# Optimization experiments

Hardware: AMD Instinct MI355X
Metric: run time of the kernel (lower is better)

Reference implementation:

```python
import jax, jax.numpy as jnp
import numpy as np
from jax import lax

EPS = 1e-5
BETA = 0.25  # commitment cost

def _conv(x, w, b):
    y = lax.conv_general_dilated(x, w, (1, 1), 'VALID',
                                 dimension_numbers=('NCHW', 'OIHW', 'NCHW'))
    return y + b[None, :, None, None]

def _maxpool2(x):
    return lax.reduce_window(x, -jnp.inf, lax.max, (1, 1, 2, 2), (1, 1, 2, 2), 'VALID')

def _bn(x, scale, bias):
    # training-mode batch norm over (N, H, W)
    mean = jnp.mean(x, axis=(0, 2, 3), keepdims=True)
    var = jnp.var(x, axis=(0, 2, 3), keepdims=True)
    xhat = (x - mean) * lax.rsqrt(var + EPS)
    return xhat * scale[None, :, None, None] + bias[None, :, None, None]

def _vq(z_nchw, codebook):
    # z: [B,32,4,4] -> vectors [B*16, 32]
    B, C, H, W = z_nchw.shape
    z = jnp.transpose(z_nchw, (0, 2, 3, 1)).reshape(-1, C)          # [N, D]
    # squared L2 distances to codebook [K, D]
    d = (jnp.sum(z * z, axis=1, keepdims=True)
         + jnp.sum(codebook * codebook, axis=1)
         - 2.0 * z @ codebook.T)                                    # [N, K]
    idx = jnp.argmin(d, axis=1)                                     # [N]
    q = codebook[idx]                                               # [N, D]
    sg = lax.stop_gradient
    vq_loss = jnp.mean((q - sg(z)) ** 2) + BETA * jnp.mean((sg(q) - z) ** 2)
    q_st = z + sg(q - z)                                            # straight-through
    recon = jnp.transpose(q_st.reshape(B, H, W, C), (0, 3, 1, 2))
    return recon, vq_loss

def setup_inputs() -> dict:
    key = jax.random.key(0)
    ks = jax.random.split(key, 12)
    f = lambda k, shape, s: (jax.random.normal(k, shape, jnp.float32) * s)
    inp = {
        'x': jax.random.normal(ks[0], (2048, 3, 32, 32), jnp.float32),
        'conv1_w': f(ks[1], (64, 3, 3, 3), 0.1), 'conv1_b': jnp.zeros((64,), jnp.float32),
        'bn1_scale': jnp.ones((64,), jnp.float32), 'bn1_bias': jnp.zeros((64,), jnp.float32),
        'conv2_w': f(ks[2], (32, 64, 3, 3), 0.05), 'conv2_b': jnp.zeros((32,), jnp.float32),
        'bn2_scale': jnp.ones((32,), jnp.float32), 'bn2_bias': jnp.zeros((32,), jnp.float32),
        'conv3_w': f(ks[3], (32, 32, 3, 3), 0.06), 'conv3_b': jnp.zeros((32,), jnp.float32),
        'bn3_scale': jnp.ones((32,), jnp.float32), 'bn3_bias': jnp.zeros((32,), jnp.float32),
        'codebook': f(ks[4], (100, 32), 0.5),
        'fc1_w': f(ks[5], (64, 512), 0.04), 'fc1_b': jnp.zeros((64,), jnp.float32),
        'fc2_w': f(ks[6], (10, 64), 0.12), 'fc2_b': jnp.zeros((10,), jnp.float32),
    }
    return inp

def reference(x, conv1_w, conv1_b, bn1_scale, bn1_bias,
              conv2_w, conv2_b, bn2_scale, bn2_bias,
              conv3_w, conv3_b, bn3_scale, bn3_bias,
              codebook, fc1_w, fc1_b, fc2_w, fc2_b):
    h = _bn(jax.nn.relu(_maxpool2(_conv(x, conv1_w, conv1_b))), bn1_scale, bn1_bias)
    h = _bn(jax.nn.relu(_maxpool2(_conv(h, conv2_w, conv2_b))), bn2_scale, bn2_bias)
    h = _bn(jax.nn.relu(_conv(h, conv3_w, conv3_b)), bn3_scale, bn3_bias)   # [B,32,4,4]
    recon, vq_loss = _vq(h, codebook)
    blended = 0.5 * recon + h
    flat = blended.reshape(-1, 4 * 4 * 32)
    z1 = jax.nn.relu(flat @ fc1_w.T + fc1_b)
    y = z1 @ fc2_w.T + fc2_b
    return recon, h, vq_loss, jax.nn.log_softmax(y, axis=1)
```

## Files before the change

kernel.cpp:

```cpp
#include <hip/hip_runtime.h>
#include <math.h>


#define CNT1 460800.0
#define CNT2 73728.0
#define CNT3 32768.0

template<int CB, int W4, int J0, int CNT>
__device__ __forceinline__ void conv1_seg(const float* img, const float* wr,
                                          int prow, float bias, float* vout)
{
  float acc[CNT][4];
#pragma unroll
  for (int j = 0; j < CNT; ++j) { acc[j][0] = 0; acc[j][1] = 0; acc[j][2] = 0; acc[j][3] = 0; }
#pragma unroll
  for (int cin = 0; cin < 3; ++cin) {
    float pt[4][4 * W4];
    const float4* src = (const float4*)&img[cin * 1024 + (2 * prow) * 32 + CB];
#pragma unroll
    for (int r = 0; r < 4; ++r)
#pragma unroll
      for (int u = 0; u < W4; ++u) {
        float4 f = src[r * 8 + u];
        pt[r][u * 4 + 0] = f.x; pt[r][u * 4 + 1] = f.y;
        pt[r][u * 4 + 2] = f.z; pt[r][u * 4 + 3] = f.w;
      }
#pragma unroll
    for (int jj = 0; jj < CNT; ++jj) {
      const int c0 = 2 * (J0 + jj) - CB;
#pragma unroll
      for (int kh = 0; kh < 3; ++kh)
#pragma unroll
        for (int kw = 0; kw < 3; ++kw) {
          const float w_ = wr[cin * 9 + kh * 3 + kw];
          acc[jj][0] += pt[kh][c0 + kw] * w_;
          acc[jj][1] += pt[kh][c0 + 1 + kw] * w_;
          acc[jj][2] += pt[kh + 1][c0 + kw] * w_;
          acc[jj][3] += pt[kh + 1][c0 + 1 + kw] * w_;
        }
    }
  }
#pragma unroll
  for (int jj = 0; jj < CNT; ++jj) {
    float v = fmaxf(fmaxf(acc[jj][0], acc[jj][1]), fmaxf(acc[jj][2], acc[jj][3])) + bias;
    vout[J0 + jj] = fmaxf(v, 0.f);
  }
}

__global__ __launch_bounds__(256) void k1_conv1(
    const float* __restrict__ x, const float* __restrict__ w1,
    const float* __restrict__ b1, double* __restrict__ dstats,
    float* __restrict__ y1)
{
  __shared__ float img[3072];
  __shared__ float red_s[256], red_q[256];
  const int n = blockIdx.x, t = threadIdx.x;
  const float4* xin = (const float4*)(x + n * 3072);
  float4* img4 = (float4*)img;
  for (int i = t; i < 768; i += 256) img4[i] = xin[i];
  const int ch = t & 63, rslot = t >> 6;
  float wr[27];
#pragma unroll
  for (int k = 0; k < 27; ++k) wr[k] = w1[ch * 27 + k];
  const float bias = b1[ch];
  __syncthreads();
  float s = 0.f, ss = 0.f;
  for (int prow = rslot; prow < 15; prow += 4) {
    float vout[15];
    conv1_seg<0, 4, 0, 7>(img, wr, prow, bias, vout);
    conv1_seg<12, 4, 7, 5>(img, wr, prow, bias, vout);
    conv1_seg<24, 2, 12, 3>(img, wr, prow, bias, vout);
    float4* dst = (float4*)(y1 + n * 15360 + ch * 240 + prow * 16);
    dst[0] = make_float4(vout[0], vout[1], vout[2], vout[3]);
    dst[1] = make_float4(vout[4], vout[5], vout[6], vout[7]);
    dst[2] = make_float4(vout[8], vout[9], vout[10], vout[11]);
    dst[3] = make_float4(vout[12], vout[13], vout[14], 0.f);
#pragma unroll
    for (int j = 0; j < 15; ++j) { s += vout[j]; ss += vout[j] * vout[j]; }
  }
  red_s[t] = s; red_q[t] = ss;
  __syncthreads();
  if (t < 64) {
    float rs = red_s[t] + red_s[t + 64] + red_s[t + 128] + red_s[t + 192];
    float rq = red_q[t] + red_q[t + 64] + red_q[t + 128] + red_q[t + 192];
    atomicAdd(&dstats[t * 16], (double)rs);
    atomicAdd(&dstats[t * 16 + 8], (double)rq);
  }
}

__global__ __launch_bounds__(256) void k1_conv1_stats(
    const float* __restrict__ x, const float* __restrict__ w1,
    const float* __restrict__ b1, double* __restrict__ dstats)
{
  __shared__ float img[3072];
  __shared__ float red[512];
  const int n = blockIdx.x, t = threadIdx.x;
  const float4* xin = (const float4*)(x + n * 3072);
  float4* img4 = (float4*)img;
  for (int i = t; i < 768; i += 256) img4[i] = xin[i];
  const int c = t >> 2, q = t & 3;
  float wr[27];
#pragma unroll
  for (int k = 0; k < 27; ++k) wr[k] = w1[c * 27 + k];
  const float bias = b1[c];
  __syncthreads();
  float s = 0.f, ss = 0.f;
  for (int p = q; p < 225; p += 4) {
    const int i = p / 15, j = p % 15;
    float a0 = 0, a1 = 0, a2 = 0, a3 = 0;
#pragma unroll
    for (int cin = 0; cin < 3; ++cin) {
      float pt[4][4];
#pragma unroll
      for (int r = 0; r < 4; ++r) {
        const float2* row = (const float2*)&img[cin * 1024 + (2 * i + r) * 32 + 2 * j];
        float2 u = row[0], v = row[1];
        pt[r][0] = u.x; pt[r][1] = u.y; pt[r][2] = v.x; pt[r][3] = v.y;
      }
#pragma unroll
      for (int kh = 0; kh < 3; ++kh)
#pragma unroll
        for (int kw = 0; kw < 3; ++kw) {
          const float wv = wr[cin * 9 + kh * 3 + kw];
          a0 += pt[kh][kw] * wv;     a1 += pt[kh][kw + 1] * wv;
          a2 += pt[kh + 1][kw] * wv; a3 += pt[kh + 1][kw + 1] * wv;
        }
    }
    float v = fmaxf(fmaxf(a0, a1), fmaxf(a2, a3)) + bias;
    v = fmaxf(v, 0.f);
    s += v; ss += v * v;
  }
  red[t * 2] = s; red[t * 2 + 1] = ss;
  __syncthreads();
  if (q == 0) {
    float rs = red[t * 2] + red[(t + 1) * 2] + red[(t + 2) * 2] + red[(t + 3) * 2];
    float rq = red[t * 2 + 1] + red[(t + 1) * 2 + 1] + red[(t + 2) * 2 + 1] + red[(t + 3) * 2 + 1];
    atomicAdd(&dstats[c * 16], (double)rs);
    atomicAdd(&dstats[c * 16 + 8], (double)rq);
  }
}

__global__ void k_finalize(const double* __restrict__ dstats,
                           const float* __restrict__ scale, const float* __restrict__ bias,
                           float* __restrict__ a, float* __restrict__ b, int C, double inv_cnt)
{
  int c = threadIdx.x;
  if (c < C) {
    double mean = dstats[c * 16] * inv_cnt;
    double var = dstats[c * 16 + 8] * inv_cnt - mean * mean;
    double ai = (double)scale[c] / sqrt(var + 1e-5);
    a[c] = (float)ai;
    b[c] = (float)((double)bias[c] - mean * ai);
  }
}

__global__ void k2b_prep(const float* __restrict__ w2, const float* __restrict__ b2,
                         const float* __restrict__ bn1s, const float* __restrict__ bn1b,
                         const double* __restrict__ dstats,
                         float* __restrict__ w2s, float* __restrict__ b2eff)
{
  const int idx = blockIdx.x * 256 + threadIdx.x;
  const int half = idx & 1, cog = (idx >> 1) & 15;
  const int r = (idx >> 5) % 72, cc = idx / 2304;
  const int o = cog + 16 * half;
  const int ci = cc * 8 + r / 9, s = r % 9;
  {
    double mean = dstats[ci * 16] / CNT1;
    double var = dstats[ci * 16 + 8] / CNT1 - mean * mean;
    float ai = (float)((double)bn1s[ci] / sqrt(var + 1e-5));
    w2s[idx] = w2[o * 576 + ci * 9 + s] * ai;
  }
  if (blockIdx.x == 0 && threadIdx.x < 32) {
    const int co = threadIdx.x;
    float c = b2[co];
    for (int cj = 0; cj < 64; ++cj) {
      double mean = dstats[cj * 16] / CNT1;
      double var = dstats[cj * 16 + 8] / CNT1 - mean * mean;
      double ai = (double)bn1s[cj] / sqrt(var + 1e-5);
      float bf = (float)((double)bn1b[cj] - mean * ai);
      float wsum = 0.f;
#pragma unroll
      for (int s2 = 0; s2 < 9; ++s2) wsum += w2[co * 576 + cj * 9 + s2];
      c += bf * wsum;
    }
    b2eff[co] = c;
  }
}

__global__ __launch_bounds__(384) void k3_conv2_fast(
    const float* __restrict__ y1, const float* __restrict__ w2s,
    const float* __restrict__ b2eff, float* __restrict__ y2,
    double* __restrict__ dstats2)
{
  __shared__ float y1n[4 * 1928];
  __shared__ float w2c[72 * 32];
  __shared__ float sum2L[32], ss2L[32];
  const int t = threadIdx.x;
  const int n0 = blockIdx.x * 4;
  if (t < 32) { sum2L[t] = 0.f; ss2L[t] = 0.f; }
  const int irow = t / 64;
  const int img = (t >> 4) & 3;
  const int cog = t & 15;

  float acc[2][6][4];
#pragma unroll
  for (int h = 0; h < 2; ++h)
#pragma unroll
    for (int j = 0; j < 6; ++j) { acc[h][j][0] = 0; acc[h][j][1] = 0; acc[h][j][2] = 0; acc[h][j][3] = 0; }

  for (int cc = 0; cc < 8; ++cc) {
    __syncthreads();
    for (int idx = t; idx < 1920; idx += 384) {
      const int im = idx / 480, wi = idx - im * 480;
      ((float4*)y1n)[im * 482 + wi] =
          ((const float4*)(y1 + (n0 + im) * 15360 + cc * 1920))[wi];
    }
    for (int idx = t; idx < 576; idx += 384)
      ((float4*)w2c)[idx] = ((const float4*)(w2s + cc * 2304))[idx];
    __syncthreads();
    for (int ci = 0; ci < 8; ++ci) {
      float wv0[9], wv1[9];
#pragma unroll
      for (int s = 0; s < 9; ++s) {
        float2 wp = *(const float2*)&w2c[(ci * 9 + s) * 32 + cog * 2];
        wv0[s] = wp.x; wv1[s] = wp.y;
      }
      float pt[4][16];
      const float4* src = (const float4*)&y1n[img * 1928 + ci * 240 + 2 * irow * 16];
#pragma unroll
      for (int r = 0; r < 4; ++r)
#pragma unroll
        for (int u = 0; u < 4; ++u) {
          float4 f = src[r * 4 + u];
          pt[r][u * 4 + 0] = f.x; pt[r][u * 4 + 1] = f.y;
          pt[r][u * 4 + 2] = f.z; pt[r][u * 4 + 3] = f.w;
        }
#pragma unroll
      for (int j = 0; j < 6; ++j)
#pragma unroll
        for (int kh = 0; kh < 3; ++kh)
#pragma unroll
          for (int kw = 0; kw < 3; ++kw) {
            const float p00 = pt[kh][2 * j + kw],     p01 = pt[kh][2 * j + 1 + kw];
            const float p10 = pt[kh + 1][2 * j + kw], p11 = pt[kh + 1][2 * j + 1 + kw];
            const float w0 = wv0[kh * 3 + kw], w1_ = wv1[kh * 3 + kw];
            acc[0][j][0] += p00 * w0;  acc[0][j][1] += p01 * w0;
            acc[0][j][2] += p10 * w0;  acc[0][j][3] += p11 * w0;
            acc[1][j][0] += p00 * w1_; acc[1][j][1] += p01 * w1_;
            acc[1][j][2] += p10 * w1_; acc[1][j][3] += p11 * w1_;
          }
    }
  }
  const int n = n0 + img;
#pragma unroll
  for (int half = 0; half < 2; ++half) {
    const int co = cog + half * 16;
    const float bias = b2eff[co];
    float s = 0.f, sq = 0.f;
#pragma unroll
    for (int j = 0; j < 6; ++j) {
      float v = fmaxf(fmaxf(acc[half][j][0], acc[half][j][1]),
                      fmaxf(acc[half][j][2], acc[half][j][3])) + bias;
      v = fmaxf(v, 0.f);
      y2[n * 1152 + co * 36 + irow * 6 + j] = v;
      s += v; sq += v * v;
    }
    atomicAdd(&sum2L[co], s);
    atomicAdd(&ss2L[co], sq);
  }
  __syncthreads();
  if (t < 32) {
    atomicAdd(&dstats2[t * 16], (double)sum2L[t]);
    atomicAdd(&dstats2[t * 16 + 8], (double)ss2L[t]);
  }
}

__global__ __launch_bounds__(256) void k3_conv2(
    const float* __restrict__ x, const float* __restrict__ w1,
    const float* __restrict__ b1, const float* __restrict__ a1f,
    const float* __restrict__ b1f, const float* __restrict__ w2,
    const float* __restrict__ b2, float* __restrict__ y2,
    double* __restrict__ dstats2)
{
  __shared__ float img[3072];
  __shared__ float y1n[16 * 240];
  __shared__ float w2c[144 * 32];
  __shared__ float sum2L[32], ss2L[32];
  const int n = blockIdx.x, t = threadIdx.x;
  if (t < 32) { sum2L[t] = 0.f; ss2L[t] = 0.f; }
  const float4* xin = (const float4*)(x + n * 3072);
  float4* img4 = (float4*)img;
  for (int i = t; i < 768; i += 256) img4[i] = xin[i];

  const int co = t & 31, irow = t >> 5;
  const bool activeC = (irow < 6);

  float acc[6][4];
#pragma unroll
  for (int j = 0; j < 6; ++j) { acc[j][0] = 0; acc[j][1] = 0; acc[j][2] = 0; acc[j][3] = 0; }

  const int cA = t >> 4, qA = t & 15;

  for (int cc = 0; cc < 4; ++cc) {
    __syncthreads();
    {
      const int ch = cc * 16 + cA;
      float wr[27];
#pragma unroll
      for (int k = 0; k < 27; ++k) wr[k] = w1[ch * 27 + k];
      const float bias = b1[ch];
      const float an = a1f[ch], bn = b1f[ch];
      for (int p = qA; p < 225; p += 16) {
        const int i = p / 15, j = p % 15;
        float a0 = 0, a1 = 0, a2 = 0, a3 = 0;
#pragma unroll
        for (int cin = 0; cin < 3; ++cin) {
          float pt[4][4];
#pragma unroll
          for (int r = 0; r < 4; ++r) {
            const float2* row = (const float2*)&img[cin * 1024 + (2 * i + r) * 32 + 2 * j];
            float2 u = row[0], v = row[1];
            pt[r][0] = u.x; pt[r][1] = u.y; pt[r][2] = v.x; pt[r][3] = v.y;
          }
#pragma unroll
          for (int kh = 0; kh < 3; ++kh)
#pragma unroll
            for (int kw = 0; kw < 3; ++kw) {
              const float wv = wr[cin * 9 + kh * 3 + kw];
              a0 += pt[kh][kw] * wv;     a1 += pt[kh][kw + 1] * wv;
              a2 += pt[kh + 1][kw] * wv; a3 += pt[kh + 1][kw + 1] * wv;
            }
        }
        float v = fmaxf(fmaxf(a0, a1), fmaxf(a2, a3)) + bias;
        v = fmaxf(v, 0.f);
        y1n[cA * 240 + i * 16 + j] = an * v + bn;
      }
    }
    for (int idx = t; idx < 4608; idx += 256) {
      const int o = idx & 31, r = idx >> 5;
      w2c[r * 32 + o] = w2[o * 576 + cc * 144 + r];
    }
    __syncthreads();
    if (activeC) {
      for (int ci = 0; ci < 16; ++ci) {
        float wv[9];
#pragma unroll
        for (int s = 0; s < 9; ++s) wv[s] = w2c[(ci * 9 + s) * 32 + co];
        float pt[4][16];
        const float4* src = (const float4*)&y1n[ci * 240 + (2 * irow) * 16];
#pragma unroll
        for (int r = 0; r < 4; ++r)
#pragma unroll
          for (int u = 0; u < 4; ++u) {
            float4 f = src[r * 4 + u];
            pt[r][u * 4] = f.x; pt[r][u * 4 + 1] = f.y;
            pt[r][u * 4 + 2] = f.z; pt[r][u * 4 + 3] = f.w;
          }
#pragma unroll
        for (int j = 0; j < 6; ++j) {
#pragma unroll
          for (int kh = 0; kh < 3; ++kh)
#pragma unroll
            for (int kw = 0; kw < 3; ++kw) {
              const float w_ = wv[kh * 3 + kw];
              acc[j][0] += pt[kh][2 * j + kw] * w_;
              acc[j][1] += pt[kh][2 * j + 1 + kw] * w_;
              acc[j][2] += pt[kh + 1][2 * j + kw] * w_;
              acc[j][3] += pt[kh + 1][2 * j + 1 + kw] * w_;
            }
        }
      }
    }
  }
  if (activeC) {
    const float bias = b2[co];
    float s = 0.f, sq = 0.f;
#pragma unroll
    for (int j = 0; j < 6; ++j) {
      float v = fmaxf(fmaxf(acc[j][0], acc[j][1]), fmaxf(acc[j][2], acc[j][3])) + bias;
      v = fmaxf(v, 0.f);
      y2[n * 1152 + co * 36 + irow * 6 + j] = v;
      s += v; sq += v * v;
    }
    atomicAdd(&sum2L[co], s);
    atomicAdd(&ss2L[co], sq);
  }
  __syncthreads();
  if (t < 32) {
    atomicAdd(&dstats2[t * 16], (double)sum2L[t]);
    atomicAdd(&dstats2[t * 16 + 8], (double)ss2L[t]);
  }
}

__global__ __launch_bounds__(256) void k5_conv3(
    const float* __restrict__ y2, const double* __restrict__ dstats2,
    const float* __restrict__ bn2s, const float* __restrict__ bn2b,
    const float* __restrict__ w3, const float* __restrict__ b3,
    float* __restrict__ t3, double* __restrict__ dstats3)
{
  __shared__ float y2n[8 * 1152];
  __shared__ float w3c[144 * 32];
  __shared__ float a2s[32], b2s[32];
  __shared__ float sum3L[32], ss3L[32];
  const int blk = blockIdx.x, t = threadIdx.x;
  if (t < 32) {
    sum3L[t] = 0.f; ss3L[t] = 0.f;
    double mean = dstats2[t * 16] / CNT2;
    double var = dstats2[t * 16 + 8] / CNT2 - mean * mean;
    double ai = (double)bn2s[t] / sqrt(var + 1e-5);
    a2s[t] = (float)ai;
    b2s[t] = (float)((double)bn2b[t] - mean * ai);
  }
  __syncthreads();
  for (int idx = t; idx < 9216; idx += 256) {
    const int ci = (idx % 1152) / 36;
    y2n[idx] = a2s[ci] * y2[blk * 9216 + idx] + b2s[ci];
  }
  const int il = t >> 5, c = t & 31;
  float acc[16];
#pragma unroll
  for (int p = 0; p < 16; ++p) acc[p] = 0.f;
  for (int ch = 0; ch < 2; ++ch) {
    __syncthreads();
    for (int idx = t; idx < 4608; idx += 256) {
      const int o = idx & 31, r = idx >> 5;
      w3c[r * 32 + o] = w3[o * 288 + ch * 144 + r];
    }
    __syncthreads();
    for (int ci = 0; ci < 16; ++ci) {
      float wv[9];
#pragma unroll
      for (int s = 0; s < 9; ++s) wv[s] = w3c[(ci * 9 + s) * 32 + c];
      float pt[36];
      const float4* src = (const float4*)&y2n[il * 1152 + (ch * 16 + ci) * 36];
#pragma unroll
      for (int u = 0; u < 9; ++u) {
        float4 f = src[u];
        pt[u * 4] = f.x; pt[u * 4 + 1] = f.y; pt[u * 4 + 2] = f.z; pt[u * 4 + 3] = f.w;
      }
#pragma unroll
      for (int i = 0; i < 4; ++i)
#pragma unroll
        for (int j = 0; j < 4; ++j) {
          float a_ = 0.f;
#pragma unroll
          for (int kh = 0; kh < 3; ++kh)
#pragma unroll
            for (int kw = 0; kw < 3; ++kw)
              a_ += pt[(i + kh) * 6 + j + kw] * wv[kh * 3 + kw];
          acc[i * 4 + j] += a_;
        }
    }
  }
  const float bias = b3[c];
  float s = 0.f, sq = 0.f;
  float vout[16];
#pragma unroll
  for (int p = 0; p < 16; ++p) {
    float v = fmaxf(acc[p] + bias, 0.f);
    vout[p] = v; s += v; sq += v * v;
  }
  const int n = blk * 8 + il;
  float4* dst = (float4*)&t3[(n * 32 + c) * 16];
#pragma unroll
  for (int u = 0; u < 4; ++u)
    dst[u] = make_float4(vout[u * 4], vout[u * 4 + 1], vout[u * 4 + 2], vout[u * 4 + 3]);
  atomicAdd(&sum3L[c], s);
  atomicAdd(&ss3L[c], sq);
  __syncthreads();
  if (t < 32) {
    atomicAdd(&dstats3[t * 16], (double)sum3L[t]);
    atomicAdd(&dstats3[t * 16 + 8], (double)ss3L[t]);
  }
}

__global__ __launch_bounds__(256) void k8_vq(
    const float* __restrict__ t3, const double* __restrict__ dstats3,
    const float* __restrict__ bn3s, const float* __restrict__ bn3b,
    const float* __restrict__ cbg, float* __restrict__ recon,
    float* __restrict__ hout, double* __restrict__ dloss)
{
  __shared__ float cb[3200];
  __shared__ float n2[100];
  __shared__ float a3s[32], b3s[32];
  const int t = threadIdx.x;
  for (int i = t; i < 3200; i += 256) cb[i] = cbg[i];
  if (t < 32) {
    double mean = dstats3[t * 16] / CNT3;
    double var = dstats3[t * 16 + 8] / CNT3 - mean * mean;
    double ai = (double)bn3s[t] / sqrt(var + 1e-5);
    a3s[t] = (float)ai;
    b3s[t] = (float)((double)bn3b[t] - mean * ai);
  }
  __syncthreads();
  if (t < 100) {
    float s = 0.f;
#pragma unroll
    for (int c = 0; c < 32; ++c) { float v = cb[t * 32 + c]; s += v * v; }
    n2[t] = s;
  }
  __syncthreads();
  const int v = blockIdx.x * 256 + t;
  const int b = v >> 4, p = v & 15;
  float z[32];
  float z2 = 0.f;
#pragma unroll
  for (int c = 0; c < 32; ++c) {
    const float zz = a3s[c] * t3[b * 512 + c * 16 + p] + b3s[c];
    hout[b * 512 + c * 16 + p] = zz;
    z[c] = zz; z2 += zz * zz;
  }
  float best = 1e30f; int bi = 0;
  for (int k = 0; k < 100; ++k) {
    float dot = 0.f;
#pragma unroll
    for (int c = 0; c < 32; ++c) dot += z[c] * cb[k * 32 + c];
    const float d = z2 + n2[k] - 2.f * dot;
    if (d < best) { best = d; bi = k; }
  }
  float lsum = 0.f;
#pragma unroll
  for (int c = 0; c < 32; ++c) {
    const float qv = cb[bi * 32 + c];
    recon[b * 512 + c * 16 + p] = qv;
    const float df = qv - z[c];
    lsum += df * df;
  }
#pragma unroll
  for (int off = 32; off > 0; off >>= 1) lsum += __shfl_down(lsum, off, 64);
  if ((t & 63) == 0) atomicAdd(dloss, (double)lsum);
}

__global__ __launch_bounds__(256) void k10_fc(
    const float* __restrict__ recon, const float* __restrict__ h,
    const float* __restrict__ fc1w, const float* __restrict__ fc1b,
    const float* __restrict__ fc2w, const float* __restrict__ fc2b,
    float* __restrict__ out, const double* __restrict__ dloss,
    float* __restrict__ loss_out)
{
  __shared__ float flat[4 * 512];
  __shared__ float z1[4 * 64];
  __shared__ float yL[4 * 10];
  const int t = threadIdx.x;
  const int w = t >> 6, l = t & 63;
  const int n = blockIdx.x * 4 + w;
  if (blockIdx.x == 0 && t == 0)
    loss_out[0] = (float)(1.25 * dloss[0] / (32768.0 * 32.0));
  for (int k = l; k < 512; k += 64)
    flat[w * 512 + k] = 0.5f * recon[n * 512 + k] + h[n * 512 + k];
  __syncthreads();
  float acc = fc1b[l];
  const float4* wrow = (const float4*)(fc1w + l * 512);
  const float4* frow = (const float4*)(flat + w * 512);
  for (int k4 = 0; k4 < 128; ++k4) {
    const float4 wv = wrow[k4], fv = frow[k4];
    acc += wv.x * fv.x + wv.y * fv.y + wv.z * fv.z + wv.w * fv.w;
  }
  z1[w * 64 + l] = fmaxf(acc, 0.f);
  __syncthreads();
  if (l < 10) {
    float a = fc2b[l];
#pragma unroll
    for (int i = 0; i < 64; ++i) a += fc2w[l * 64 + i] * z1[w * 64 + i];
    yL[w * 10 + l] = a;
  }
  __syncthreads();
  if (l < 10) {
    float m = -1e30f;
#pragma unroll
    for (int i = 0; i < 10; ++i) m = fmaxf(m, yL[w * 10 + i]);
    float s = 0.f;
#pragma unroll
    for (int i = 0; i < 10; ++i) s += expf(yL[w * 10 + i] - m);
    out[n * 10 + l] = yL[w * 10 + l] - m - logf(s);
  }
}

extern "C" void kernel_launch(void* const* d_in, const int* in_sizes, int n_in,
                              void* d_out, int out_size, void* d_ws, size_t ws_size,
                              hipStream_t stream)
{
  (void)in_sizes; (void)n_in; (void)out_size;
  const float* x    = (const float*)d_in[0];
  const float* w1   = (const float*)d_in[1];
  const float* cb1  = (const float*)d_in[2];
  const float* bn1s = (const float*)d_in[3];
  const float* bn1b = (const float*)d_in[4];
  const float* w2   = (const float*)d_in[5];
  const float* cb2  = (const float*)d_in[6];
  const float* bn2s = (const float*)d_in[7];
  const float* bn2b = (const float*)d_in[8];
  const float* w3   = (const float*)d_in[9];
  const float* cb3  = (const float*)d_in[10];
  const float* bn3s = (const float*)d_in[11];
  const float* bn3b = (const float*)d_in[12];
  const float* cbk  = (const float*)d_in[13];
  const float* fc1w = (const float*)d_in[14];
  const float* fc1b = (const float*)d_in[15];
  const float* fc2w = (const float*)d_in[16];
  const float* fc2b = (const float*)d_in[17];
  float* out = (float*)d_out;

  double* dstats = (double*)d_ws;
  float* fws = (float*)((char*)d_ws + 32768);
  float* a1 = fws;        float* b1 = fws + 64;
  float* b2eff = fws + 128;

  float* recon_out = out;
  float* h_out     = out + 1048576;
  float* loss_out  = out + 2097152;
  float* y_out     = out + 2097153;

  const bool fast = ws_size >= 139568128ull;

  hipMemsetAsync(d_ws, 0, 32768, stream);

  if (fast) {
    float* w2s = fws + 256;
    float* y2  = fws + 256 + 18432;
    float* t3  = y2 + 2359296;
    float* y1  = t3 + 1048576;

    k1_conv1<<<2048, 256, 0, stream>>>(x, w1, cb1, dstats, y1);
    k2b_prep<<<72, 256, 0, stream>>>(w2, cb2, bn1s, bn1b, dstats, w2s, b2eff);
    k3_conv2_fast<<<512, 384, 0, stream>>>(y1, w2s, b2eff, y2, dstats + 1024);
    k5_conv3<<<256, 256, 0, stream>>>(y2, dstats + 1024, bn2s, bn2b, w3, cb3, t3, dstats + 1536);
    k8_vq<<<128, 256, 0, stream>>>(t3, dstats + 1536, bn3s, bn3b, cbk, recon_out, h_out, dstats + 2048);
    k10_fc<<<512, 256, 0, stream>>>(recon_out, h_out, fc1w, fc1b, fc2w, fc2b,
                                    y_out, dstats + 2048, loss_out);
  } else {
    float* y2 = fws + 256;
    float* t3 = fws + 256 + 2359296;

    k1_conv1_stats<<<2048, 256, 0, stream>>>(x, w1, cb1, dstats);
    k_finalize<<<1, 64, 0, stream>>>(dstats, bn1s, bn1b, a1, b1, 64, 1.0 / CNT1);
    k3_conv2<<<2048, 256, 0, stream>>>(x, w1, cb1, a1, b1, w2, cb2, y2, dstats + 1024);
    k5_conv3<<<256, 256, 0, stream>>>(y2, dstats + 1024, bn2s, bn2b, w3, cb3, t3, dstats + 1536);
    k8_vq<<<128, 256, 0, stream>>>(t3, dstats + 1536, bn3s, bn3b, cbk, recon_out, h_out, dstats + 2048);
    k10_fc<<<512, 256, 0, stream>>>(recon_out, h_out, fc1w, fc1b, fc2w, fc2b,
                                    y_out, dstats + 2048, loss_out);
  }
}
```

Measured before the change: 481.5 us.

## Split conv2 input-channel reduction across half-waves and double grid size

The conv2 kernel now processes 2 images per block instead of 4. Each 64-lane wave is split into two halves that each accumulate 4 of the 8 input channels per chunk, and the halves are combined with a cross-lane shuffle before the epilogue. This doubles the block count to raise parallelism and occupancy on the many-CU GPU, at the cost of extra shuffles and idle lanes in the epilogue. The bias-folding prep also spreads its 64-channel loop over 8 thread groups and reduces them in shared memory, instead of one 32-thread serial loop.

```diff
diff --git a/kernel.cpp b/kernel.cpp
--- a/kernel.cpp
+++ b/kernel.cpp
@@ -170,10 +170,11 @@
     float ai = (float)((double)bn1s[ci] / sqrt(var + 1e-5));
     w2s[idx] = w2[o * 576 + ci * 9 + s] * ai;
   }
-  if (blockIdx.x == 0 && threadIdx.x < 32) {
-    const int co = threadIdx.x;
-    float c = b2[co];
-    for (int cj = 0; cj < 64; ++cj) {
+  if (blockIdx.x == 0) {
+    __shared__ float part[8][32];
+    const int co = threadIdx.x & 31, g = threadIdx.x >> 5;
+    float c = 0.f;
+    for (int cj = g * 8; cj < g * 8 + 8; ++cj) {
       double mean = dstats[cj * 16] / CNT1;
       double var = dstats[cj * 16 + 8] / CNT1 - mean * mean;
       double ai = (double)bn1s[cj] / sqrt(var + 1e-5);
@@ -183,7 +184,14 @@
       for (int s2 = 0; s2 < 9; ++s2) wsum += w2[co * 576 + cj * 9 + s2];
       c += bf * wsum;
     }
-    b2eff[co] = c;
+    part[g][co] = c;
+    __syncthreads();
+    if (g == 0) {
+      float tot = b2[co];
+#pragma unroll
+      for (int k = 0; k < 8; ++k) tot += part[k][co];
+      b2eff[co] = tot;
+    }
   }
 }
 
@@ -192,15 +200,17 @@
     const float* __restrict__ b2eff, float* __restrict__ y2,
     double* __restrict__ dstats2)
 {
-  __shared__ float y1n[4 * 1928];
+  __shared__ float y1n[2 * 1928];
   __shared__ float w2c[72 * 32];
   __shared__ float sum2L[32], ss2L[32];
   const int t = threadIdx.x;
-  const int n0 = blockIdx.x * 4;
+  const int n0 = blockIdx.x * 2;
   if (t < 32) { sum2L[t] = 0.f; ss2L[t] = 0.f; }
-  const int irow = t / 64;
-  const int img = (t >> 4) & 3;
-  const int cog = t & 15;
+  const int irow = t >> 6;
+  const int l = t & 63;
+  const int ciH = l >> 5;
+  const int img = (l >> 4) & 1;
+  const int cog = l & 15;
 
   float acc[2][6][4];
 #pragma unroll
@@ -210,7 +220,7 @@
 
   for (int cc = 0; cc < 8; ++cc) {
     __syncthreads();
-    for (int idx = t; idx < 1920; idx += 384) {
+    for (int idx = t; idx < 960; idx += 384) {
       const int im = idx / 480, wi = idx - im * 480;
       ((float4*)y1n)[im * 482 + wi] =
           ((const float4*)(y1 + (n0 + im) * 15360 + cc * 1920))[wi];
@@ -218,7 +228,9 @@
     for (int idx = t; idx < 576; idx += 384)
       ((float4*)w2c)[idx] = ((const float4*)(w2s + cc * 2304))[idx];
     __syncthreads();
-    for (int ci = 0; ci < 8; ++ci) {
+#pragma unroll
+    for (int q = 0; q < 4; ++q) {
+      const int ci = ciH * 4 + q;
       float wv0[9], wv1[9];
 #pragma unroll
       for (int s = 0; s < 9; ++s) {
@@ -251,22 +263,31 @@
           }
     }
   }
-  const int n = n0 + img;
-#pragma unroll
-  for (int half = 0; half < 2; ++half) {
-    const int co = cog + half * 16;
-    const float bias = b2eff[co];
-    float s = 0.f, sq = 0.f;
-#pragma unroll
-    for (int j = 0; j < 6; ++j) {
-      float v = fmaxf(fmaxf(acc[half][j][0], acc[half][j][1]),
-                      fmaxf(acc[half][j][2], acc[half][j][3])) + bias;
-      v = fmaxf(v, 0.f);
-      y2[n * 1152 + co * 36 + irow * 6 + j] = v;
-      s += v; sq += v * v;
-    }
-    atomicAdd(&sum2L[co], s);
-    atomicAdd(&ss2L[co], sq);
+#pragma unroll
+  for (int h = 0; h < 2; ++h)
+#pragma unroll
+    for (int j = 0; j < 6; ++j)
+#pragma unroll
+      for (int p = 0; p < 4; ++p)
+        acc[h][j][p] += __shfl_xor(acc[h][j][p], 32, 64);
+  if (ciH == 0) {
+    const int n = n0 + img;
+#pragma unroll
+    for (int half = 0; half < 2; ++half) {
+      const int co = cog + half * 16;
+      const float bias = b2eff[co];
+      float s = 0.f, sq = 0.f;
+#pragma unroll
+      for (int j = 0; j < 6; ++j) {
+        float v = fmaxf(fmaxf(acc[half][j][0], acc[half][j][1]),
+                        fmaxf(acc[half][j][2], acc[half][j][3])) + bias;
+        v = fmaxf(v, 0.f);
+        y2[n * 1152 + co * 36 + irow * 6 + j] = v;
+        s += v; sq += v * v;
+      }
+      atomicAdd(&sum2L[co], s);
+      atomicAdd(&ss2L[co], sq);
+    }
   }
   __syncthreads();
   if (t < 32) {
@@ -623,7 +644,7 @@
 
     k1_conv1<<<2048, 256, 0, stream>>>(x, w1, cb1, dstats, y1);
     k2b_prep<<<72, 256, 0, stream>>>(w2, cb2, bn1s, bn1b, dstats, w2s, b2eff);
-    k3_conv2_fast<<<512, 384, 0, stream>>>(y1, w2s, b2eff, y2, dstats + 1024);
+    k3_conv2_fast<<<1024, 384, 0, stream>>>(y1, w2s, b2eff, y2, dstats + 1024);
     k5_conv3<<<256, 256, 0, stream>>>(y2, dstats + 1024, bn2s, bn2b, w3, cb3, t3, dstats + 1536);
     k8_vq<<<128, 256, 0, stream>>>(t3, dstats + 1536, bn3s, bn3b, cbk, recon_out, h_out, dstats + 2048);
     k10_fc<<<512, 256, 0, stream>>>(recon_out, h_out, fc1w, fc1b, fc2w, fc2b,
```

Result: slower. 505.4 us (+5.0%).

## Split conv3 and VQ work across more threads, read conv1 input directly

Applied to the files above, without the earlier changes.

conv3 now has each block handle 4 images, with each thread computing half the output rows, so the grid doubles to 512 blocks. VQ now uses two threads per vector, each scanning half the codebook, and merges the argmin with a shuffle that keeps the lower index on ties. The conv2 bias-fold prep spreads its 64-channel loop over 8 thread groups and reduces the partials in shared memory. conv1 drops its LDS staging of the image and reads the input from global memory directly, which saves a barrier but relies on the cache for reuse.

```diff
diff --git a/kernel.cpp b/kernel.cpp
--- a/kernel.cpp
+++ b/kernel.cpp
@@ -52,18 +52,14 @@
     const float* __restrict__ b1, double* __restrict__ dstats,
     float* __restrict__ y1)
 {
-  __shared__ float img[3072];
   __shared__ float red_s[256], red_q[256];
   const int n = blockIdx.x, t = threadIdx.x;
-  const float4* xin = (const float4*)(x + n * 3072);
-  float4* img4 = (float4*)img;
-  for (int i = t; i < 768; i += 256) img4[i] = xin[i];
+  const float* img = x + n * 3072;
   const int ch = t & 63, rslot = t >> 6;
   float wr[27];
 #pragma unroll
   for (int k = 0; k < 27; ++k) wr[k] = w1[ch * 27 + k];
   const float bias = b1[ch];
-  __syncthreads();
   float s = 0.f, ss = 0.f;
   for (int prow = rslot; prow < 15; prow += 4) {
     float vout[15];
@@ -170,10 +166,11 @@
     float ai = (float)((double)bn1s[ci] / sqrt(var + 1e-5));
     w2s[idx] = w2[o * 576 + ci * 9 + s] * ai;
   }
-  if (blockIdx.x == 0 && threadIdx.x < 32) {
-    const int co = threadIdx.x;
-    float c = b2[co];
-    for (int cj = 0; cj < 64; ++cj) {
+  if (blockIdx.x == 0) {
+    __shared__ float part[8][32];
+    const int co = threadIdx.x & 31, g = threadIdx.x >> 5;
+    float c = 0.f;
+    for (int cj = g * 8; cj < g * 8 + 8; ++cj) {
       double mean = dstats[cj * 16] / CNT1;
       double var = dstats[cj * 16 + 8] / CNT1 - mean * mean;
       double ai = (double)bn1s[cj] / sqrt(var + 1e-5);
@@ -183,7 +180,14 @@
       for (int s2 = 0; s2 < 9; ++s2) wsum += w2[co * 576 + cj * 9 + s2];
       c += bf * wsum;
     }
-    b2eff[co] = c;
+    part[g][co] = c;
+    __syncthreads();
+    if (g == 0) {
+      float tot = b2[co];
+#pragma unroll
+      for (int k = 0; k < 8; ++k) tot += part[k][co];
+      b2eff[co] = tot;
+    }
   }
 }
 
@@ -398,7 +402,7 @@
     const float* __restrict__ w3, const float* __restrict__ b3,
     float* __restrict__ t3, double* __restrict__ dstats3)
 {
-  __shared__ float y2n[8 * 1152];
+  __shared__ float y2n[4 * 1152];
   __shared__ float w3c[144 * 32];
   __shared__ float a2s[32], b2s[32];
   __shared__ float sum3L[32], ss3L[32];
@@ -412,14 +416,14 @@
     b2s[t] = (float)((double)bn2b[t] - mean * ai);
   }
   __syncthreads();
-  for (int idx = t; idx < 9216; idx += 256) {
+  for (int idx = t; idx < 4608; idx += 256) {
     const int ci = (idx % 1152) / 36;
-    y2n[idx] = a2s[ci] * y2[blk * 9216 + idx] + b2s[ci];
-  }
-  const int il = t >> 5, c = t & 31;
-  float acc[16];
-#pragma unroll
-  for (int p = 0; p < 16; ++p) acc[p] = 0.f;
+    y2n[idx] = a2s[ci] * y2[blk * 4608 + idx] + b2s[ci];
+  }
+  const int g = t >> 5, img = g & 3, ph = g >> 2, c = t & 31;
+  float acc[8];
+#pragma unroll
+  for (int p = 0; p < 8; ++p) acc[p] = 0.f;
   for (int ch = 0; ch < 2; ++ch) {
     __syncthreads();
     for (int idx = t; idx < 4608; idx += 256) {
@@ -431,15 +435,15 @@
       float wv[9];
 #pragma unroll
       for (int s = 0; s < 9; ++s) wv[s] = w3c[(ci * 9 + s) * 32 + c];
-      float pt[36];
-      const float4* src = (const float4*)&y2n[il * 1152 + (ch * 16 + ci) * 36];
-#pragma unroll
-      for (int u = 0; u < 9; ++u) {
+      float pt[24];
+      const float4* src = (const float4*)&y2n[img * 1152 + (ch * 16 + ci) * 36 + ph * 12];
+#pragma unroll
+      for (int u = 0; u < 6; ++u) {
         float4 f = src[u];
         pt[u * 4] = f.x; pt[u * 4 + 1] = f.y; pt[u * 4 + 2] = f.z; pt[u * 4 + 3] = f.w;
       }
 #pragma unroll
-      for (int i = 0; i < 4; ++i)
+      for (int i2 = 0; i2 < 2; ++i2)
 #pragma unroll
         for (int j = 0; j < 4; ++j) {
           float a_ = 0.f;
@@ -447,24 +451,23 @@
           for (int kh = 0; kh < 3; ++kh)
 #pragma unroll
             for (int kw = 0; kw < 3; ++kw)
-              a_ += pt[(i + kh) * 6 + j + kw] * wv[kh * 3 + kw];
-          acc[i * 4 + j] += a_;
+              a_ += pt[(i2 + kh) * 6 + j + kw] * wv[kh * 3 + kw];
+          acc[i2 * 4 + j] += a_;
         }
     }
   }
   const float bias = b3[c];
   float s = 0.f, sq = 0.f;
-  float vout[16];
-#pragma unroll
-  for (int p = 0; p < 16; ++p) {
+  float vout[8];
+#pragma unroll
+  for (int p = 0; p < 8; ++p) {
     float v = fmaxf(acc[p] + bias, 0.f);
     vout[p] = v; s += v; sq += v * v;
   }
-  const int n = blk * 8 + il;
-  float4* dst = (float4*)&t3[(n * 32 + c) * 16];
-#pragma unroll
-  for (int u = 0; u < 4; ++u)
-    dst[u] = make_float4(vout[u * 4], vout[u * 4 + 1], vout[u * 4 + 2], vout[u * 4 + 3]);
+  const int n = blk * 4 + img;
+  float4* dst = (float4*)&t3[(n * 32 + c) * 16 + ph * 8];
+  dst[0] = make_float4(vout[0], vout[1], vout[2], vout[3]);
+  dst[1] = make_float4(vout[4], vout[5], vout[6], vout[7]);
   atomicAdd(&sum3L[c], s);
   atomicAdd(&ss3L[c], sq);
   __syncthreads();
@@ -500,27 +503,32 @@
     n2[t] = s;
   }
   __syncthreads();
-  const int v = blockIdx.x * 256 + t;
-  const int b = v >> 4, p = v & 15;
+  const int vv = blockIdx.x * 128 + (t >> 1);
+  const int half = t & 1;
+  const int b = vv >> 4, p = vv & 15;
   float z[32];
   float z2 = 0.f;
 #pragma unroll
   for (int c = 0; c < 32; ++c) {
     const float zz = a3s[c] * t3[b * 512 + c * 16 + p] + b3s[c];
-    hout[b * 512 + c * 16 + p] = zz;
+    if ((c >> 4) == half) hout[b * 512 + c * 16 + p] = zz;
     z[c] = zz; z2 += zz * zz;
   }
-  float best = 1e30f; int bi = 0;
-  for (int k = 0; k < 100; ++k) {
+  float best = 1e30f; int bi = half * 50;
+  for (int k = half * 50; k < half * 50 + 50; ++k) {
     float dot = 0.f;
 #pragma unroll
     for (int c = 0; c < 32; ++c) dot += z[c] * cb[k * 32 + c];
     const float d = z2 + n2[k] - 2.f * dot;
     if (d < best) { best = d; bi = k; }
   }
+  const float obest = __shfl_xor(best, 1, 64);
+  const int obi = __shfl_xor(bi, 1, 64);
+  if (half ? (obest <= best) : (obest < best)) { best = obest; bi = obi; }
   float lsum = 0.f;
 #pragma unroll
-  for (int c = 0; c < 32; ++c) {
+  for (int c2 = 0; c2 < 16; ++c2) {
+    const int c = half * 16 + c2;
     const float qv = cb[bi * 32 + c];
     recon[b * 512 + c * 16 + p] = qv;
     const float df = qv - z[c];
@@ -624,8 +632,8 @@
     k1_conv1<<<2048, 256, 0, stream>>>(x, w1, cb1, dstats, y1);
     k2b_prep<<<72, 256, 0, stream>>>(w2, cb2, bn1s, bn1b, dstats, w2s, b2eff);
     k3_conv2_fast<<<512, 384, 0, stream>>>(y1, w2s, b2eff, y2, dstats + 1024);
-    k5_conv3<<<256, 256, 0, stream>>>(y2, dstats + 1024, bn2s, bn2b, w3, cb3, t3, dstats + 1536);
-    k8_vq<<<128, 256, 0, stream>>>(t3, dstats + 1536, bn3s, bn3b, cbk, recon_out, h_out, dstats + 2048);
+    k5_conv3<<<512, 256, 0, stream>>>(y2, dstats + 1024, bn2s, bn2b, w3, cb3, t3, dstats + 1536);
+    k8_vq<<<256, 256, 0, stream>>>(t3, dstats + 1536, bn3s, bn3b, cbk, recon_out, h_out, dstats + 2048);
     k10_fc<<<512, 256, 0, stream>>>(recon_out, h_out, fc1w, fc1b, fc2w, fc2b,
                                     y_out, dstats + 2048, loss_out);
   } else {
@@ -635,8 +643,8 @@
     k1_conv1_stats<<<2048, 256, 0, stream>>>(x, w1, cb1, dstats);
     k_finalize<<<1, 64, 0, stream>>>(dstats, bn1s, bn1b, a1, b1, 64, 1.0 / CNT1);
     k3_conv2<<<2048, 256, 0, stream>>>(x, w1, cb1, a1, b1, w2, cb2, y2, dstats + 1024);
-    k5_conv3<<<256, 256, 0, stream>>>(y2, dstats + 1024, bn2s, bn2b, w3, cb3, t3, dstats + 1536);
-    k8_vq<<<128, 256, 0, stream>>>(t3, dstats + 1536, bn3s, bn3b, cbk, recon_out, h_out, dstats + 2048);
+    k5_conv3<<<512, 256, 0, stream>>>(y2, dstats + 1024, bn2s, bn2b, w3, cb3, t3, dstats + 1536);
+    k8_vq<<<256, 256, 0, stream>>>(t3, dstats + 1536, bn3s, bn3b, cbk, recon_out, h_out, dstats + 2048);
     k10_fc<<<512, 256, 0, stream>>>(recon_out, h_out, fc1w, fc1b, fc2w, fc2b,
                                     y_out, dstats + 2048, loss_out);
   }
```

Result: slower. 572.7 us (+19.0%).
